# Performance work log

Measured on AMD Instinct MI355X. Metric: run time of the kernel, lower is better.

The kernel has to match this reference:

```python
import jax, jax.numpy as jnp
import numpy as np

SCALE_FACTOR = 10.0   # activation_scale_factor
POST_ROOT = 2.0       # post_product_root


def setup_inputs() -> dict:
    key = jax.random.key(0)
    k_x, k_w, k_b = jax.random.split(key, 3)
    N, F = 2097152, 64
    input = jax.random.normal(k_x, (N, F), dtype=jnp.float32)
    # trainable weight init: uniform(-1/sqrt(F), 1/sqrt(F)); avoid exact zeros not needed here
    bound = 1.0 / np.sqrt(F)
    weight = jax.random.uniform(k_w, (F,), dtype=jnp.float32, minval=-bound, maxval=bound)
    bias = jax.random.normal(k_b, (F,), dtype=jnp.float32) * 0.01
    return {"input": input, "weight": weight, "bias": bias}


def reference(input, weight, bias):
    # matmul with diag(weight) is just an elementwise per-feature scale
    targets = input * weight + bias                      # [N, F]
    targets = jax.nn.sigmoid(SCALE_FACTOR * targets)     # [N, F]
    targets = targets ** (1.0 / POST_ROOT)               # [N, F]
    return jnp.prod(targets, axis=1)                     # [N]
```

## Files before the change

kernel.cpp:

```cpp
#include <hip/hip_runtime.h>
#include <hip/hip_bf16.h>


__device__ __forceinline__ float fast_exp2(float x) {
#if __has_builtin(__builtin_amdgcn_exp2f)
    return __builtin_amdgcn_exp2f(x);
#else
    return exp2f(x);
#endif
}

__device__ __forceinline__ float fast_rsqrt(float x) {
#if __has_builtin(__builtin_amdgcn_rsqf)
    return __builtin_amdgcn_rsqf(x);
#else
    return rsqrtf(x);
#endif
}

__global__ __launch_bounds__(256) void one2one_prod_kernel(
    const float* __restrict__ in,
    const float* __restrict__ w,
    const float* __restrict__ b,
    float* __restrict__ out,
    long long total_f4)
{
    const float NEG10LOG2E = -10.0f * 1.44269504088896340736f;
    const int grp = threadIdx.x & 15;
    const int c0 = grp * 4;

    const float4 wv = *(const float4*)(w + c0);
    const float4 bv = *(const float4*)(b + c0);
    const float a0 = NEG10LOG2E * wv.x, a1 = NEG10LOG2E * wv.y;
    const float a2 = NEG10LOG2E * wv.z, a3 = NEG10LOG2E * wv.w;
    const float d0 = NEG10LOG2E * bv.x, d1 = NEG10LOG2E * bv.y;
    const float d2 = NEG10LOG2E * bv.z, d3 = NEG10LOG2E * bv.w;

    const float4* __restrict__ in4 = (const float4*)in;
    const long long stride = (long long)gridDim.x * blockDim.x;

    for (long long f = (long long)blockIdx.x * blockDim.x + threadIdx.x;
         f < total_f4; f += stride) {
        float4 x = in4[f];

        float e0 = fast_exp2(fmaf(x.x, a0, d0));
        float e1 = fast_exp2(fmaf(x.y, a1, d1));
        float e2 = fast_exp2(fmaf(x.z, a2, d2));
        float e3 = fast_exp2(fmaf(x.w, a3, d3));

        float r0 = fast_rsqrt(1.0f + e0);
        float r1 = fast_rsqrt(1.0f + e1);
        float r2 = fast_rsqrt(1.0f + e2);
        float r3 = fast_rsqrt(1.0f + e3);

        float p = (r0 * r1) * (r2 * r3);

        p *= __shfl_xor(p, 1, 64);
        p *= __shfl_xor(p, 2, 64);
        p *= __shfl_xor(p, 4, 64);
        p *= __shfl_xor(p, 8, 64);

        if (grp == 0) {
            out[f >> 4] = p;
        }
    }
}

extern "C" void kernel_launch(void* const* d_in, const int* in_sizes, int n_in,
                              void* d_out, int out_size, void* d_ws, size_t ws_size,
                              hipStream_t stream) {
    const float* in = (const float*)d_in[0];
    const float* w  = (const float*)d_in[1];
    const float* b  = (const float*)d_in[2];
    float* out = (float*)d_out;

    const long long total_f4 = (long long)in_sizes[0] / 4;

    const int block = 256;
    const int grid = 8192;
    hipLaunchKernelGGL(one2one_prod_kernel, dim3(grid), dim3(block), 0, stream,
                       in, w, b, out, total_f4);
}
```

Baseline: 674.8 us.

## Fold per-element rsqrt into one rsqrt of product, swizzle reduction, unroll loads

```diff
diff --git a/kernel.cpp b/kernel.cpp
--- a/kernel.cpp
+++ b/kernel.cpp
@@ -1,83 +1,90 @@
 #include <hip/hip_runtime.h>
-#include <hip/hip_bf16.h>
 
 
-__device__ __forceinline__ float fast_exp2(float x) {
-#if __has_builtin(__builtin_amdgcn_exp2f)
-    return __builtin_amdgcn_exp2f(x);
-#else
-    return exp2f(x);
-#endif
+typedef float vfloat4 __attribute__((ext_vector_type(4)));
+
+__device__ __forceinline__ float exp2_hw(float x) {
+    float r; asm("v_exp_f32 %0, %1" : "=v"(r) : "v"(x)); return r;
+}
+__device__ __forceinline__ float rsq_hw(float x) {
+    float r; asm("v_rsq_f32 %0, %1" : "=v"(r) : "v"(x)); return r;
 }
 
-__device__ __forceinline__ float fast_rsqrt(float x) {
-#if __has_builtin(__builtin_amdgcn_rsqf)
-    return __builtin_amdgcn_rsqf(x);
-#else
-    return rsqrtf(x);
-#endif
+template <int PAT>
+__device__ __forceinline__ float bfly_mul(float p) {
+    int q = __builtin_amdgcn_ds_swizzle(__builtin_bit_cast(int, p), PAT);
+    return p * __builtin_bit_cast(float, q);
+}
+__device__ __forceinline__ float group16_prod(float p) {
+    p = bfly_mul<0x041F>(p);
+    p = bfly_mul<0x081F>(p);
+    p = bfly_mul<0x101F>(p);
+    p = bfly_mul<0x201F>(p);
+    return p;
 }
 
 __global__ __launch_bounds__(256) void one2one_prod_kernel(
-    const float* __restrict__ in,
-    const float* __restrict__ w,
-    const float* __restrict__ b,
-    float* __restrict__ out,
-    long long total_f4)
+    const vfloat4* __restrict__ in4,
+    const float*   __restrict__ w,
+    const float*   __restrict__ b,
+    float*         __restrict__ out,
+    int total_f4)
 {
-    const float NEG10LOG2E = -10.0f * 1.44269504088896340736f;
+    const float C = -14.4269504088896340736f;
     const int grp = threadIdx.x & 15;
-    const int c0 = grp * 4;
 
-    const float4 wv = *(const float4*)(w + c0);
-    const float4 bv = *(const float4*)(b + c0);
-    const float a0 = NEG10LOG2E * wv.x, a1 = NEG10LOG2E * wv.y;
-    const float a2 = NEG10LOG2E * wv.z, a3 = NEG10LOG2E * wv.w;
-    const float d0 = NEG10LOG2E * bv.x, d1 = NEG10LOG2E * bv.y;
-    const float d2 = NEG10LOG2E * bv.z, d3 = NEG10LOG2E * bv.w;
+    const vfloat4 wv = ((const vfloat4*)w)[grp];
+    const vfloat4 bv = ((const vfloat4*)b)[grp];
+    const float a0 = C * wv.x, a1 = C * wv.y, a2 = C * wv.z, a3 = C * wv.w;
+    const float d0 = C * bv.x, d1 = C * bv.y, d2 = C * bv.z, d3 = C * bv.w;
 
-    const float4* __restrict__ in4 = (const float4*)in;
-    const long long stride = (long long)gridDim.x * blockDim.x;
+    const int stride = gridDim.x * blockDim.x;
+    int f = blockIdx.x * blockDim.x + threadIdx.x;
 
-    for (long long f = (long long)blockIdx.x * blockDim.x + threadIdx.x;
-         f < total_f4; f += stride) {
-        float4 x = in4[f];
+    for (; f + stride < total_f4; f += 2 * stride) {
+        vfloat4 x = __builtin_nontemporal_load(&in4[f]);
+        vfloat4 y = __builtin_nontemporal_load(&in4[f + stride]);
 
-        float e0 = fast_exp2(fmaf(x.x, a0, d0));
-        float e1 = fast_exp2(fmaf(x.y, a1, d1));
-        float e2 = fast_exp2(fmaf(x.z, a2, d2));
-        float e3 = fast_exp2(fmaf(x.w, a3, d3));
+        float px = (1.0f + exp2_hw(fmaf(x.x, a0, d0)))
+                 * (1.0f + exp2_hw(fmaf(x.y, a1, d1)))
+                 * (1.0f + exp2_hw(fmaf(x.z, a2, d2)))
+                 * (1.0f + exp2_hw(fmaf(x.w, a3, d3)));
+        float py = (1.0f + exp2_hw(fmaf(y.x, a0, d0)))
+                 * (1.0f + exp2_hw(fmaf(y.y, a1, d1)))
+                 * (1.0f + exp2_hw(fmaf(y.z, a2, d2)))
+                 * (1.0f + exp2_hw(fmaf(y.w, a3, d3)));
 
-        float r0 = fast_rsqrt(1.0f + e0);
-        float r1 = fast_rsqrt(1.0f + e1);
-        float r2 = fast_rsqrt(1.0f + e2);
-        float r3 = fast_rsqrt(1.0f + e3);
-
-        float p = (r0 * r1) * (r2 * r3);
-
-        p *= __shfl_xor(p, 1, 64);
-        p *= __shfl_xor(p, 2, 64);
-        p *= __shfl_xor(p, 4, 64);
-        p *= __shfl_xor(p, 8, 64);
+        px = group16_prod(px);
+        py = group16_prod(py);
 
         if (grp == 0) {
-            out[f >> 4] = p;
+            out[f >> 4]            = rsq_hw(px);
+            out[(f + stride) >> 4] = rsq_hw(py);
         }
+    }
+    if (f < total_f4) {
+        vfloat4 x = __builtin_nontemporal_load(&in4[f]);
+        float px = (1.0f + exp2_hw(fmaf(x.x, a0, d0)))
+                 * (1.0f + exp2_hw(fmaf(x.y, a1, d1)))
+                 * (1.0f + exp2_hw(fmaf(x.z, a2, d2)))
+                 * (1.0f + exp2_hw(fmaf(x.w, a3, d3)));
+        px = group16_prod(px);
+        if (grp == 0) out[f >> 4] = rsq_hw(px);
     }
 }
 
 extern "C" void kernel_launch(void* const* d_in, const int* in_sizes, int n_in,
                               void* d_out, int out_size, void* d_ws, size_t ws_size,
                               hipStream_t stream) {
-    const float* in = (const float*)d_in[0];
-    const float* w  = (const float*)d_in[1];
-    const float* b  = (const float*)d_in[2];
+    const vfloat4* in4 = (const vfloat4*)d_in[0];
+    const float*   w   = (const float*)d_in[1];
+    const float*   b   = (const float*)d_in[2];
     float* out = (float*)d_out;
 
-    const long long total_f4 = (long long)in_sizes[0] / 4;
+    const int total_f4 = in_sizes[0] / 4;
 
     const int block = 256;
-    const int grid = 8192;
+    const int grid  = 8192;
     hipLaunchKernelGGL(one2one_prod_kernel, dim3(grid), dim3(block), 0, stream,
-                       in, w, b, out, total_f4);
+                       in4, w, b, out, total_f4);
 }
```

After: 666.7 us. No clear change (-1.2%).
